# Kernel optimization log

Measured on AMD Instinct MI355X. Metric: run time of the kernel, lower is better.

Reference implementation:

```python
import jax, jax.numpy as jnp
import numpy as np

TEMP = 0.1
ALPHA = 0.5
REG_W = 0.1
DTW_BETA = 0.1
DTW_SCALE = 10.0

BS, D, NF, NC = 128, 768, 64, 32


def _l2norm(x, eps=1e-12):
    return x / jnp.maximum(jnp.linalg.norm(x, axis=-1, keepdims=True), eps)


def _ce_diag(logits):
    # cross-entropy with targets = arange(n): positives on the diagonal
    lsm = jax.nn.log_softmax(logits, axis=-1)
    return -jnp.mean(jnp.diagonal(lsm))


def clip_info_ce(v, t, temp=TEMP):
    # CLIP-style symmetric InfoNCE on L2-normalized embeddings
    v = _l2norm(v)
    t = _l2norm(t)
    logits = (v @ t.T) / temp
    return 0.5 * (_ce_diag(logits) + _ce_diag(logits.T))


def ntxent(v, t, temp=TEMP, alpha=ALPHA):
    # SimCLR-style NT-Xent over the 2N concatenated views, alpha-weighted per direction
    n = v.shape[0]
    z = _l2norm(jnp.concatenate([v, t], axis=0))  # [2n, d]
    sim = (z @ z.T) / temp
    sim = jnp.where(jnp.eye(2 * n, dtype=bool), -1e9, sim)  # mask self-similarity
    lsm = jax.nn.log_softmax(sim, axis=-1)
    pos_idx = jnp.concatenate([jnp.arange(n) + n, jnp.arange(n)])
    pos = lsm[jnp.arange(2 * n), pos_idx]
    return alpha * (-jnp.mean(pos[:n])) + (1.0 - alpha) * (-jnp.mean(pos[n:]))


def _softmin3(a, b, c, beta):
    x = jnp.stack([a, b, c], axis=0)
    return -beta * jax.nn.logsumexp(-x / beta, axis=0)


def soft_dtw(cost, beta):
    # cost: [P, N, M] -> soft-DTW distance [P] via anti-causal DP (scan rows, scan cols)
    row0 = jnp.cumsum(cost[:, 0, :], axis=-1)  # [P, M], only-right path on first row

    def row_step(R_prev, cost_row):  # R_prev, cost_row: [P, M]
        r_first = cost_row[:, 0] + R_prev[:, 0]  # only-up move at j=0

        def col_step(r_left, inp):
            c, up, diag = inp  # each [P]
            r = c + _softmin3(r_left, up, diag, beta)
            return r, r

        xs = (cost_row[:, 1:].T, R_prev[:, 1:].T, R_prev[:, :-1].T)  # [M-1, P]
        _, rest = jax.lax.scan(col_step, r_first, xs)
        R_row = jnp.concatenate([r_first[None, :], rest], axis=0).T  # [P, M]
        return R_row, None

    R_last, _ = jax.lax.scan(row_step, row0, jnp.swapaxes(cost[:, 1:, :], 0, 1))
    return R_last[:, -1]


def dtw_contrastive_loss(embs_v, embs_t, beta=DTW_BETA, scale=DTW_SCALE):
    # embs_v: [B, F, D] (normalized), embs_t: [B, C, D] (normalized)
    B, Fn, _ = embs_v.shape
    C = embs_t.shape[1]
    sim = jnp.einsum('bfd,gcd->bgfc', embs_v, embs_t)  # all-pairs frame/token sims
    cost = 1.0 - sim
    D_mat = soft_dtw(cost.reshape(B * B, Fn, C), beta).reshape(B, B)
    logits = -scale * D_mat  # smaller alignment cost -> larger logit
    return 0.5 * (_ce_diag(logits) + _ce_diag(logits.T))


def setup_inputs() -> dict:
    key = jax.random.key(0)
    k1, k2, k3, k4, k5 = jax.random.split(key, 5)
    return {
        'video_embd': jax.random.normal(k1, (BS, D), dtype=jnp.float32),
        'text_embd_sent': jax.random.normal(k2, (BS, D), dtype=jnp.float32),
        'text_embd_cand': jax.random.normal(k3, (BS, NC, D), dtype=jnp.float32),
        'video_embd_frame': jax.random.normal(k4, (BS, NF, D), dtype=jnp.float32),
        'pos_step': jax.random.randint(k5, (BS,), 0, NC, dtype=jnp.int64 if jax.config.jax_enable_x64 else jnp.int32),
    }


def reference(video_embd, text_embd_sent, text_embd_cand, video_embd_frame, pos_step):
    loss_1 = clip_info_ce(video_embd, text_embd_sent)
    loss_2 = ntxent(video_embd, text_embd_sent)
    aggregate_text = jnp.mean(text_embd_cand, axis=1)
    loss_3 = clip_info_ce(video_embd, aggregate_text)
    loss_4 = clip_info_ce(text_embd_sent, aggregate_text)
    embs_v = _l2norm(video_embd_frame)
    embs_t = _l2norm(text_embd_cand)
    loss_dtw = dtw_contrastive_loss(embs_v, embs_t)
    return (loss_1 + loss_2 + loss_3 + loss_4 + REG_W * loss_dtw) / 5.0
```

## Files before the change

kernel.cpp:

```cpp
#include <hip/hip_runtime.h>
#include <stdint.h>

typedef unsigned short ushort_t;
typedef __attribute__((ext_vector_type(4))) float f32x4;
typedef __attribute__((ext_vector_type(8))) short short8;
typedef __attribute__((ext_vector_type(4))) ushort_t us4;
typedef __attribute__((ext_vector_type(4))) int i32x4;
typedef __attribute__((ext_vector_type(8))) int i32x8;

#define LDS_AS __attribute__((address_space(3)))
#define GLB_AS __attribute__((address_space(1)))

__device__ __forceinline__ ushort_t f2bf(float f) {
    uint32_t u = __float_as_uint(f);
    u += 0x7FFFu + ((u >> 16) & 1u);
    return (ushort_t)(u >> 16);
}

__device__ __forceinline__ float bf2f(ushort_t u) {
    return __uint_as_float(((uint32_t)u) << 16);
}

__device__ __forceinline__ float dpp_shr1z(float x) {
    return __int_as_float(__builtin_amdgcn_update_dpp(
        0, __float_as_int(x), 0x138, 0xF, 0xF, false));
}

__device__ __forceinline__ uint32_t pk_fp8(float4 x) {
    int u = __builtin_amdgcn_cvt_pk_fp8_f32(x.x, x.y, 0, false);
    u = __builtin_amdgcn_cvt_pk_fp8_f32(x.z, x.w, u, true);
    return (uint32_t)u;
}

__global__ __launch_bounds__(256) void k_prep_all(
    const float* __restrict__ frame, const float* __restrict__ cand,
    const float* __restrict__ video, const float* __restrict__ sent,
    uint8_t* __restrict__ A8, uint8_t* __restrict__ B8, ushort_t* __restrict__ Zbf,
    float* __restrict__ P)
{
    if (blockIdx.x == 0) {
        for (int i = threadIdx.x; i < 1152; i += 256) P[i] = 0.0f;
    }
    const int w = threadIdx.x >> 6, ln = threadIdx.x & 63;
    const int r = blockIdx.x * 4 + w;
    float4 x0, x1, x2;
    bool isfp8 = (r < 12288);
    uint8_t* dst8 = nullptr;
    ushort_t* dstz = nullptr;
    if (r < 8192) {
        const float4* s = (const float4*)(frame + (size_t)r * 768);
        x0 = s[ln]; x1 = s[ln + 64]; x2 = s[ln + 128];
        dst8 = A8 + (size_t)r * 768;
    } else if (r < 12288) {
        int q = r - 8192;
        const float4* s = (const float4*)(cand + (size_t)q * 768);
        x0 = s[ln]; x1 = s[ln + 64]; x2 = s[ln + 128];
        dst8 = B8 + (size_t)q * 768;
    } else if (r < 12416) {
        int q = r - 12288;
        const float4* s = (const float4*)(video + (size_t)q * 768);
        x0 = s[ln]; x1 = s[ln + 64]; x2 = s[ln + 128];
        dstz = Zbf + (size_t)q * 768;
    } else if (r < 12544) {
        int q = r - 12416;
        const float4* s = (const float4*)(sent + (size_t)q * 768);
        x0 = s[ln]; x1 = s[ln + 64]; x2 = s[ln + 128];
        dstz = Zbf + (size_t)(128 + q) * 768;
    } else {
        int b = r - 12544;
        x0 = x1 = x2 = make_float4(0.f, 0.f, 0.f, 0.f);
        for (int k = 0; k < 32; ++k) {
            const float4* s = (const float4*)(cand + (size_t)(b * 32 + k) * 768);
            float4 y0 = s[ln], y1 = s[ln + 64], y2 = s[ln + 128];
            x0.x += y0.x; x0.y += y0.y; x0.z += y0.z; x0.w += y0.w;
            x1.x += y1.x; x1.y += y1.y; x1.z += y1.z; x1.w += y1.w;
            x2.x += y2.x; x2.y += y2.y; x2.z += y2.z; x2.w += y2.w;
        }
        const float s32 = 1.0f / 32.0f;
        x0.x *= s32; x0.y *= s32; x0.z *= s32; x0.w *= s32;
        x1.x *= s32; x1.y *= s32; x1.z *= s32; x1.w *= s32;
        x2.x *= s32; x2.y *= s32; x2.z *= s32; x2.w *= s32;
        dstz = Zbf + (size_t)(256 + b) * 768;
    }
    float ss = x0.x*x0.x + x0.y*x0.y + x0.z*x0.z + x0.w*x0.w
             + x1.x*x1.x + x1.y*x1.y + x1.z*x1.z + x1.w*x1.w
             + x2.x*x2.x + x2.y*x2.y + x2.z*x2.z + x2.w*x2.w;
    #pragma unroll
    for (int off = 32; off > 0; off >>= 1) ss += __shfl_xor(ss, off);
    float sc = 1.0f / fmaxf(sqrtf(ss), 1e-12f);
    x0.x *= sc; x0.y *= sc; x0.z *= sc; x0.w *= sc;
    x1.x *= sc; x1.y *= sc; x1.z *= sc; x1.w *= sc;
    x2.x *= sc; x2.y *= sc; x2.z *= sc; x2.w *= sc;
    if (isfp8) {
        uint32_t* d32 = (uint32_t*)dst8;
        d32[ln] = pk_fp8(x0); d32[ln + 64] = pk_fp8(x1); d32[ln + 128] = pk_fp8(x2);
    } else {
        us4 u0, u1, u2;
        u0.x = f2bf(x0.x); u0.y = f2bf(x0.y); u0.z = f2bf(x0.z); u0.w = f2bf(x0.w);
        u1.x = f2bf(x1.x); u1.y = f2bf(x1.y); u1.z = f2bf(x1.z); u1.w = f2bf(x1.w);
        u2.x = f2bf(x2.x); u2.y = f2bf(x2.y); u2.z = f2bf(x2.z); u2.w = f2bf(x2.w);
        us4* d4 = (us4*)dstz;
        d4[ln] = u0; d4[ln + 64] = u1; d4[ln + 128] = u2;
    }
}

__global__ __launch_bounds__(256, 4) void k_fused(
    const uint8_t* __restrict__ A, const uint8_t* __restrict__ B,
    const ushort_t* __restrict__ Z,
    float* __restrict__ G, float* __restrict__ P, float* __restrict__ Dm)
{
    __shared__ __align__(16) ushort_t lds[16384];
    const int t = threadIdx.x;
    const int lane = t & 63, w = t >> 6;
    const int lr = lane & 15, lk = lane >> 4;

    if (blockIdx.x < 9) {
        ushort_t* As = lds;
        ushort_t* Bs = lds + 8192;
        const int bx = blockIdx.x;
        const int m0 = (bx / 3) * 128, n0 = (bx % 3) * 128;
        const int wr = w >> 1, wc = w & 1;
        f32x4 acc[4][4] = {};
        for (int k0 = 0; k0 < 768; k0 += 64) {
            #pragma unroll
            for (int ii = 0; ii < 4; ++ii) {
                int idx = ii * 256 + t;
                int row = idx >> 3, kc = (idx & 7) * 8;
                __builtin_amdgcn_global_load_lds(
                    (const GLB_AS void*)(Z + (size_t)(m0 + row) * 768 + (k0 + kc)),
                    (LDS_AS void*)(As + idx * 8), 16, 0, 0);
            }
            #pragma unroll
            for (int ii = 0; ii < 4; ++ii) {
                int idx = ii * 256 + t;
                int row = idx >> 3, kc = (idx & 7) * 8;
                __builtin_amdgcn_global_load_lds(
                    (const GLB_AS void*)(Z + (size_t)(n0 + row) * 768 + (k0 + kc)),
                    (LDS_AS void*)(Bs + idx * 8), 16, 0, 0);
            }
            __syncthreads();
            #pragma unroll
            for (int kk = 0; kk < 2; ++kk) {
                short8 av[4], bv[4];
                #pragma unroll
                for (int f = 0; f < 4; ++f)
                    av[f] = *(const short8*)(As + (wr * 64 + f * 16 + lr) * 64 + kk * 32 + lk * 8);
                #pragma unroll
                for (int f = 0; f < 4; ++f)
                    bv[f] = *(const short8*)(Bs + (wc * 64 + f * 16 + lr) * 64 + kk * 32 + lk * 8);
                #pragma unroll
                for (int fr = 0; fr < 4; ++fr)
                    #pragma unroll
                    for (int fc = 0; fc < 4; ++fc)
                        acc[fr][fc] = __builtin_amdgcn_mfma_f32_16x16x32_bf16(av[fr], bv[fc], acc[fr][fc], 0, 0, 0);
            }
            __syncthreads();
        }
        #pragma unroll
        for (int fr = 0; fr < 4; ++fr)
            #pragma unroll
            for (int fc = 0; fc < 4; ++fc) {
                int col = n0 + wc * 64 + fc * 16 + lr;
                #pragma unroll
                for (int q = 0; q < 4; ++q) {
                    int row = m0 + wr * 64 + fr * 16 + lk * 4 + q;
                    G[(size_t)row * 384 + col] = 10.0f * acc[fr][fc][q];
                }
            }
        #pragma unroll
        for (int fr = 0; fr < 4; ++fr)
            #pragma unroll
            for (int q = 0; q < 4; ++q) {
                float e = 0.0f;
                #pragma unroll
                for (int fc = 0; fc < 4; ++fc)
                    e += expf(10.0f * acc[fr][fc][q] - 10.0f);
                #pragma unroll
                for (int off = 1; off < 16; off <<= 1) e += __shfl_xor(e, off);
                if (lr == 0) {
                    int row = m0 + wr * 64 + fr * 16 + lk * 4 + q;
                    atomicAdd(&P[row * 3 + (bx % 3)], e);
                }
            }
        return;
    }

    uint8_t* lds8 = (uint8_t*)lds;
    const int wr = w >> 1, wc = w & 1;
    const int sw = lr & 7;
    const int lin = blockIdx.x - 9;
    const int xcd = lin & 7, idx = lin >> 3;
    const int ntl = idx >> 3;
    const int mt  = xcd * 8 + (idx & 7);
    const int m0 = mt * 128, n0 = ntl * 128;

    f32x4 acc[4][4] = {};

    #pragma unroll 1
    for (int k0 = 0; k0 < 6; ++k0) {
        #pragma unroll
        for (int i = 0; i < 4; ++i) {
            int s = i * 256 + t, row = s >> 3, c16 = s & 7;
            int g = (c16 ^ (row & 7)) * 16;
            __builtin_amdgcn_global_load_lds(
                (const GLB_AS void*)(A + (size_t)(m0 + row) * 768 + k0 * 128 + g),
                (LDS_AS void*)(lds8 + s * 16), 16, 0, 0);
            __builtin_amdgcn_global_load_lds(
                (const GLB_AS void*)(B + (size_t)(n0 + row) * 768 + k0 * 128 + g),
                (LDS_AS void*)(lds8 + 16384 + s * 16), 16, 0, 0);
        }
        __syncthreads();
        i32x8 av[4];
        #pragma unroll
        for (int f = 0; f < 4; ++f) {
            const uint8_t* rb = lds8 + (wr * 64 + f * 16 + lr) * 128;
            i32x4 lo = *(const i32x4*)(rb + (((lk * 2) ^ sw) * 16));
            i32x4 hi = *(const i32x4*)(rb + (((lk * 2 + 1) ^ sw) * 16));
            av[f][0] = lo[0]; av[f][1] = lo[1]; av[f][2] = lo[2]; av[f][3] = lo[3];
            av[f][4] = hi[0]; av[f][5] = hi[1]; av[f][6] = hi[2]; av[f][7] = hi[3];
        }
        #pragma unroll
        for (int fc = 0; fc < 4; ++fc) {
            const uint8_t* rb = lds8 + 16384 + (wc * 64 + fc * 16 + lr) * 128;
            i32x4 lo = *(const i32x4*)(rb + (((lk * 2) ^ sw) * 16));
            i32x4 hi = *(const i32x4*)(rb + (((lk * 2 + 1) ^ sw) * 16));
            i32x8 bv;
            bv[0] = lo[0]; bv[1] = lo[1]; bv[2] = lo[2]; bv[3] = lo[3];
            bv[4] = hi[0]; bv[5] = hi[1]; bv[6] = hi[2]; bv[7] = hi[3];
            #pragma unroll
            for (int fr = 0; fr < 4; ++fr)
                acc[fr][fc] = __builtin_amdgcn_mfma_scale_f32_16x16x128_f8f6f4(
                    av[fr], bv, acc[fr][fc], 0, 0,
                    0, 0x7F7F7F7F, 0, 0x7F7F7F7F);
        }
        __syncthreads();
    }

    const float K10   = 14.4269504f;
    const float K10_3 = 4.80898347f;
    ushort_t* qd = lds + w * 4096;
    #pragma unroll
    for (int fr = 0; fr < 4; ++fr)
        #pragma unroll
        for (int fc = 0; fc < 4; ++fc)
            #pragma unroll
            for (int q = 0; q < 4; ++q)
                qd[(fr * 16 + lk * 4 + q) * 64 + fc * 16 + lr] =
                    f2bf(__builtin_amdgcn_exp2f(fmaf(K10, acc[fr][fc][q], -K10_3)));

    const float KD   = 785.76917f;
    const float DG0  = 1.472968e-18f;
    const float FEXT = 864.08889f;
    const int j = lane & 31, pr = lane >> 5;
    const bool isj0 = (j == 0);
    float rp = 0.0f, rp2 = 0.0f, dgj0 = DG0;

    #pragma unroll 5
    for (int s = 0; s < 95; ++s) {
        float lf  = dpp_shr1z(rp);
        float dgv = dpp_shr1z(rp2);
        if (isj0) { lf = 0.0f; dgv = dgj0; }
        int ii = s - j;
        int iic = ii < 0 ? 0 : (ii > 63 ? 63 : ii);
        float Ec = bf2f(qd[iic * 64 + lane]);
        float sum = rp + lf;
        sum = fmaf(KD, dgv, sum);
        float r = Ec * sum;
        bool act = (unsigned)ii < 64u;
        rp2 = act ? rp : rp2;
        rp  = act ? r  : rp;
        dgj0 = 0.0f;
    }
    if (j == 31) {
        int b  = mt * 2 + wr;
        int bp = ntl * 4 + wc * 2 + pr;
        Dm[(size_t)b * 128 + bp] = (FEXT - __builtin_amdgcn_logf(rp)) * (1.0f / K10);
    }
}

__global__ __launch_bounds__(256) void k_rowloss(
    const float* __restrict__ G, const float* __restrict__ P,
    const float* __restrict__ Dm, float* __restrict__ rowloss)
{
    const int w = threadIdx.x >> 6, ln = threadIdx.x & 63;
    const int i = blockIdx.x * 4 + w;
    float d1 = G[(size_t)i * 384 + 128 + i];
    float d3 = G[(size_t)i * 384 + 256 + i];
    float d4 = G[(size_t)(128 + i) * 384 + 256 + i];
    float l1 = 0.5f * ((10.0f + logf(P[i * 3 + 1]) - d1) + (10.0f + logf(P[(128 + i) * 3 + 0]) - d1));
    float l3 = 0.5f * ((10.0f + logf(P[i * 3 + 2]) - d3) + (10.0f + logf(P[(256 + i) * 3 + 0]) - d3));
    float l4 = 0.5f * ((10.0f + logf(P[(128 + i) * 3 + 2]) - d4) + (10.0f + logf(P[(256 + i) * 3 + 1]) - d4));
    float ntr = P[i * 3 + 0] + P[i * 3 + 1] - expf(G[(size_t)i * 384 + i] - 10.0f);
    float ntc = P[(128 + i) * 3 + 0] + P[(128 + i) * 3 + 1]
              - expf(G[(size_t)(128 + i) * 384 + 128 + i] - 10.0f);
    float nt = 0.5f * (10.0f + logf(ntr) - d1) + 0.5f * (10.0f + logf(ntc) - d1);
    float v0 = -10.0f * Dm[i * 128 + ln],        v1 = -10.0f * Dm[i * 128 + 64 + ln];
    float c0 = -10.0f * Dm[ln * 128 + i],        c1 = -10.0f * Dm[(64 + ln) * 128 + i];
    float mxr = fmaxf(v0, v1), mxc = fmaxf(c0, c1);
    #pragma unroll
    for (int off = 32; off > 0; off >>= 1) {
        mxr = fmaxf(mxr, __shfl_xor(mxr, off));
        mxc = fmaxf(mxc, __shfl_xor(mxc, off));
    }
    float sr = expf(v0 - mxr) + expf(v1 - mxr);
    float sc = expf(c0 - mxc) + expf(c1 - mxc);
    #pragma unroll
    for (int off = 32; off > 0; off >>= 1) {
        sr += __shfl_xor(sr, off);
        sc += __shfl_xor(sc, off);
    }
    float dd = -10.0f * Dm[i * 128 + i];
    float ld = 0.5f * ((mxr + logf(sr) - dd) + (mxc + logf(sc) - dd));
    if (ln == 0) rowloss[i] = l1 + l3 + l4 + nt + 0.1f * ld;
}

__global__ __launch_bounds__(128) void k_sum(const float* __restrict__ rowloss, float* __restrict__ out)
{
    int i = threadIdx.x;
    float tot = rowloss[i];
    #pragma unroll
    for (int o = 32; o > 0; o >>= 1) tot += __shfl_down(tot, o);
    __shared__ float sm[2];
    if ((i & 63) == 0) sm[i >> 6] = tot;
    __syncthreads();
    if (i == 0) out[0] = (sm[0] + sm[1]) / (128.0f * 5.0f);
}

extern "C" void kernel_launch(void* const* d_in, const int* in_sizes, int n_in,
                              void* d_out, int out_size, void* d_ws, size_t ws_size,
                              hipStream_t stream)
{
    (void)in_sizes; (void)n_in; (void)out_size; (void)ws_size;
    const float* video = (const float*)d_in[0];
    const float* sent  = (const float*)d_in[1];
    const float* cand  = (const float*)d_in[2];
    const float* frame = (const float*)d_in[3];

    char* ws = (char*)d_ws;
    size_t off = 0;
    auto alloc = [&](size_t b) { void* p = ws + off; off = (off + b + 255) & ~(size_t)255; return p; };
    uint8_t*  A8  = (uint8_t*)alloc((size_t)8192 * 768);
    uint8_t*  B8  = (uint8_t*)alloc((size_t)4096 * 768);
    ushort_t* Zbf = (ushort_t*)alloc((size_t)384 * 768 * 2);
    float*    G   = (float*)alloc((size_t)384 * 384 * 4);
    float*    P   = (float*)alloc((size_t)1152 * 4);
    float*    Dm  = (float*)alloc((size_t)128 * 128 * 4);
    float*    RL  = (float*)alloc((size_t)128 * 4);

    k_prep_all <<<3168, 256, 0, stream>>>(frame, cand, video, sent, A8, B8, Zbf, P);
    k_fused    <<<2057, 256, 0, stream>>>(A8, B8, Zbf, G, P, Dm);
    k_rowloss  <<<32, 256, 0, stream>>>(G, P, Dm, RL);
    k_sum      <<<1, 128, 0, stream>>>(RL, (float*)d_out);
}
```

Baseline: 72.49 us.

## Prefetch next fp8 tile into LDS while MFMAs run on register copy

Restructures the fp8 GEMM k-loop so that all A and B fragments for the current tile are loaded from LDS into registers first. The global-to-LDS load of the next tile is then issued before the MFMA block, overlapping memory transfer with compute while keeping a single LDS buffer. This needs more registers to hold all B fragments, so launch bounds drop from 4 to 3 waves per SIMD, trading occupancy for overlap.

```diff
diff --git a/kernel.cpp b/kernel.cpp
--- a/kernel.cpp
+++ b/kernel.cpp
@@ -104,7 +104,7 @@
     }
 }
 
-__global__ __launch_bounds__(256, 4) void k_fused(
+__global__ __launch_bounds__(256, 3) void k_fused(
     const uint8_t* __restrict__ A, const uint8_t* __restrict__ B,
     const ushort_t* __restrict__ Z,
     float* __restrict__ G, float* __restrict__ P, float* __restrict__ Dm)
@@ -196,45 +196,49 @@
 
     f32x4 acc[4][4] = {};
 
+#define STAGE(tile) { \
+    _Pragma("unroll") \
+    for (int i_ = 0; i_ < 4; ++i_) { \
+        int s_ = i_ * 256 + t, row_ = s_ >> 3, c16_ = s_ & 7; \
+        int g_ = (c16_ ^ (row_ & 7)) * 16; \
+        __builtin_amdgcn_global_load_lds( \
+            (const GLB_AS void*)(A + (size_t)(m0 + row_) * 768 + (tile) * 128 + g_), \
+            (LDS_AS void*)(lds8 + s_ * 16), 16, 0, 0); \
+        __builtin_amdgcn_global_load_lds( \
+            (const GLB_AS void*)(B + (size_t)(n0 + row_) * 768 + (tile) * 128 + g_), \
+            (LDS_AS void*)(lds8 + 16384 + s_ * 16), 16, 0, 0); \
+    } }
+
+    STAGE(0)
     #pragma unroll 1
     for (int k0 = 0; k0 < 6; ++k0) {
-        #pragma unroll
-        for (int i = 0; i < 4; ++i) {
-            int s = i * 256 + t, row = s >> 3, c16 = s & 7;
-            int g = (c16 ^ (row & 7)) * 16;
-            __builtin_amdgcn_global_load_lds(
-                (const GLB_AS void*)(A + (size_t)(m0 + row) * 768 + k0 * 128 + g),
-                (LDS_AS void*)(lds8 + s * 16), 16, 0, 0);
-            __builtin_amdgcn_global_load_lds(
-                (const GLB_AS void*)(B + (size_t)(n0 + row) * 768 + k0 * 128 + g),
-                (LDS_AS void*)(lds8 + 16384 + s * 16), 16, 0, 0);
+        __syncthreads();
+        i32x8 av[4], bv[4];
+        #pragma unroll
+        for (int f = 0; f < 4; ++f) {
+            const uint8_t* ra = lds8 + (wr * 64 + f * 16 + lr) * 128;
+            i32x4 alo = *(const i32x4*)(ra + (((lk * 2) ^ sw) * 16));
+            i32x4 ahi = *(const i32x4*)(ra + (((lk * 2 + 1) ^ sw) * 16));
+            av[f][0] = alo[0]; av[f][1] = alo[1]; av[f][2] = alo[2]; av[f][3] = alo[3];
+            av[f][4] = ahi[0]; av[f][5] = ahi[1]; av[f][6] = ahi[2]; av[f][7] = ahi[3];
+            const uint8_t* rb = lds8 + 16384 + (wc * 64 + f * 16 + lr) * 128;
+            i32x4 blo = *(const i32x4*)(rb + (((lk * 2) ^ sw) * 16));
+            i32x4 bhi = *(const i32x4*)(rb + (((lk * 2 + 1) ^ sw) * 16));
+            bv[f][0] = blo[0]; bv[f][1] = blo[1]; bv[f][2] = blo[2]; bv[f][3] = blo[3];
+            bv[f][4] = bhi[0]; bv[f][5] = bhi[1]; bv[f][6] = bhi[2]; bv[f][7] = bhi[3];
         }
         __syncthreads();
-        i32x8 av[4];
-        #pragma unroll
-        for (int f = 0; f < 4; ++f) {
-            const uint8_t* rb = lds8 + (wr * 64 + f * 16 + lr) * 128;
-            i32x4 lo = *(const i32x4*)(rb + (((lk * 2) ^ sw) * 16));
-            i32x4 hi = *(const i32x4*)(rb + (((lk * 2 + 1) ^ sw) * 16));
-            av[f][0] = lo[0]; av[f][1] = lo[1]; av[f][2] = lo[2]; av[f][3] = lo[3];
-            av[f][4] = hi[0]; av[f][5] = hi[1]; av[f][6] = hi[2]; av[f][7] = hi[3];
-        }
-        #pragma unroll
-        for (int fc = 0; fc < 4; ++fc) {
-            const uint8_t* rb = lds8 + 16384 + (wc * 64 + fc * 16 + lr) * 128;
-            i32x4 lo = *(const i32x4*)(rb + (((lk * 2) ^ sw) * 16));
-            i32x4 hi = *(const i32x4*)(rb + (((lk * 2 + 1) ^ sw) * 16));
-            i32x8 bv;
-            bv[0] = lo[0]; bv[1] = lo[1]; bv[2] = lo[2]; bv[3] = lo[3];
-            bv[4] = hi[0]; bv[5] = hi[1]; bv[6] = hi[2]; bv[7] = hi[3];
+        if (k0 < 5) STAGE(k0 + 1)
+        __builtin_amdgcn_sched_barrier(0);
+        #pragma unroll
+        for (int fc = 0; fc < 4; ++fc)
             #pragma unroll
             for (int fr = 0; fr < 4; ++fr)
                 acc[fr][fc] = __builtin_amdgcn_mfma_scale_f32_16x16x128_f8f6f4(
-                    av[fr], bv, acc[fr][fc], 0, 0,
+                    av[fr], bv[fc], acc[fr][fc], 0, 0,
                     0, 0x7F7F7F7F, 0, 0x7F7F7F7F);
-        }
-        __syncthreads();
-    }
+    }
+#undef STAGE
 
     const float K10   = 14.4269504f;
     const float K10_3 = 4.80898347f;
```

Result: slower. 74.59 us (+2.9%).
